# Optimization experiments

Hardware: AMD Instinct MI355X
Metric: run time of the kernel (lower is better)

Reference implementation:

```python
import jax, jax.numpy as jnp
import numpy as np

IN_SIZE = 256
OUT_SIZE = 2


def setup_inputs() -> dict:
    key = jax.random.key(0)
    k1, k2, k3, k4 = jax.random.split(key, 4)
    B, S, D, O = 32, 1024, IN_SIZE, OUT_SIZE
    input1 = jax.random.normal(k1, (B, S, D), dtype=jnp.float32)
    input2 = jax.random.normal(k2, (B, S, D), dtype=jnp.float32)
    # learned parameters
    w1 = jax.random.normal(k3, (D, O, D), dtype=jnp.float32) * 0.02
    w2 = jax.random.normal(k4, (2 * D + 1, O), dtype=jnp.float32) * 0.02
    return {"input1": input1, "input2": input2, "w1": w1, "w2": w2}


def reference(input1, input2, w1, w2):
    D = w1.shape[0]
    # bilinear term: bxi,ioj,byj -> bxyo
    logits1 = jnp.einsum('bxi,ioj,byj->bxyo', input1, w1, input2)
    # linear term: original concat([f1, f2, 1]) @ w2 == input1 @ w2[:D]
    # broadcast over y, plus input2 @ w2[D:2D] broadcast over x, plus bias w2[2D]
    lin1 = jnp.einsum('bxd,do->bxo', input1, w2[:D])        # (B, S, O)
    lin2 = jnp.einsum('byd,do->byo', input2, w2[D:2 * D])   # (B, S, O)
    bias = w2[2 * D]                                        # (O,)
    logits2 = lin1[:, :, None, :] + lin2[:, None, :, :] + bias
    return logits1 + logits2
```

## Files before the change

### kernel.cpp

```cpp
#include <hip/hip_runtime.h>
#include <hip/hip_bf16.h>
#include <cstdint>
#include <cstddef>


typedef __bf16 bf16_t;
typedef __bf16 bf16x4 __attribute__((ext_vector_type(4)));
typedef __bf16 bf16x8 __attribute__((ext_vector_type(8)));
typedef float  f32x4  __attribute__((ext_vector_type(4)));
typedef float  f32x16 __attribute__((ext_vector_type(16)));

#define NB   32
#define NS   1024
#define ND   256
#define NM   (NB * NS)
#define NN1  512

__device__ __forceinline__ void gload_lds16(const void* g, void* l) {
  __builtin_amdgcn_global_load_lds(
      (__attribute__((address_space(1))) void*)g,
      (__attribute__((address_space(3))) void*)l, 16, 0, 0);
}

__global__ __launch_bounds__(256) void prep_kernel(
    const float* __restrict__ in1, const float* __restrict__ in2,
    const float* __restrict__ w1,  const float* __restrict__ w2,
    bf16_t* __restrict__ in1b, bf16_t* __restrict__ in2b,
    bf16_t* __restrict__ w1t,  float* __restrict__ lin)
{
  int bid = blockIdx.x;
  if (bid < 16384) {
    int wave = threadIdx.x >> 6;
    int lane = threadIdx.x & 63;
    int r  = bid * 4 + wave;
    int is2 = (r >= NM) ? 1 : 0;
    int lr = r & (NM - 1);
    const float* src = is2 ? in2 : in1;
    bf16_t*      dst = is2 ? in2b : in1b;

    float4 v = *(const float4*)(src + (size_t)lr * ND + lane * 4);
    bf16x4 h;
    h[0] = (bf16_t)v.x; h[1] = (bf16_t)v.y; h[2] = (bf16_t)v.z; h[3] = (bf16_t)v.w;
    *(bf16x4*)(dst + (size_t)lr * ND + lane * 4) = h;

    int dbase = is2 * ND + lane * 4;
    float a0 = v.x * w2[(dbase + 0) * 2 + 0] + v.y * w2[(dbase + 1) * 2 + 0]
             + v.z * w2[(dbase + 2) * 2 + 0] + v.w * w2[(dbase + 3) * 2 + 0];
    float a1 = v.x * w2[(dbase + 0) * 2 + 1] + v.y * w2[(dbase + 1) * 2 + 1]
             + v.z * w2[(dbase + 2) * 2 + 1] + v.w * w2[(dbase + 3) * 2 + 1];
    #pragma unroll
    for (int off = 32; off > 0; off >>= 1) {
      a0 += __shfl_down(a0, off, 64);
      a1 += __shfl_down(a1, off, 64);
    }
    if (lane == 0) {
      if (is2) { a0 += w2[2 * ND * 2 + 0]; a1 += w2[2 * ND * 2 + 1]; }
      lin[r * 2 + 0] = a0;
      lin[r * 2 + 1] = a1;
    }
  } else {
    int wb = bid - 16384;
    int t  = threadIdx.x;
    #pragma unroll
    for (int e = 0; e < 8; ++e) {
      int q  = wb * 2048 + e * 256 + t;
      int oj = q >> 8;
      int i  = q & 255;
      w1t[q] = (bf16_t)w1[i * NN1 + oj];
    }
  }
}

__global__ __launch_bounds__(256, 3) void gemm1_kernel(
    const bf16_t* __restrict__ A, const bf16_t* __restrict__ Bt,
    bf16_t* __restrict__ T)
{
  __shared__ __align__(16) bf16_t Ap[64 * 256];
  __shared__ __align__(16) bf16_t Bc[2][128 * 32];

  int m0 = blockIdx.x * 64;
  int t = threadIdx.x, lane = t & 63, wid = t >> 6;
  int wm = (wid >> 1) * 32, wn = (wid & 1) * 64;

  #pragma unroll
  for (int i = 0; i < 8; ++i) {
    int unit = i * 256 + t;
    int row = unit >> 5;
    int c   = unit & 31;
    int cs  = c ^ (row & 7);
    gload_lds16(A + (size_t)(m0 + row) * ND + cs * 8, (char*)Ap + unit * 16);
  }
  #pragma unroll
  for (int i = 0; i < 2; ++i) {
    int unit = i * 256 + t;
    int row = unit >> 2, c = unit & 3, cs = c ^ (row & 3);
    gload_lds16(Bt + (size_t)row * ND + cs * 8, (char*)Bc[0] + unit * 16);
  }
  __syncthreads();

  f32x4 acc[2][4] = {};

  for (int s = 0; s < 32; ++s) {
    if (s + 1 < 32) {
      int nt = (s + 1) >> 3, j0 = ((s + 1) & 7) * 32;
      bf16_t* dst = (bf16_t*)Bc[(s + 1) & 1];
      #pragma unroll
      for (int i = 0; i < 2; ++i) {
        int unit = i * 256 + t;
        int row = unit >> 2, c = unit & 3, cs = c ^ (row & 3);
        gload_lds16(Bt + (size_t)(nt * 128 + row) * ND + j0 + cs * 8,
                    (char*)dst + unit * 16);
      }
    }
    const bf16_t* Bcur = Bc[s & 1];
    bf16x8 bfr[4];
    #pragma unroll
    for (int ni = 0; ni < 4; ++ni) {
      int r = wn + ni * 16 + (lane & 15);
      int cp = (lane >> 4) ^ (r & 3);
      bfr[ni] = *(const bf16x8*)&Bcur[r * 32 + cp * 8];
    }
    #pragma unroll
    for (int mi = 0; mi < 2; ++mi) {
      int r = wm + mi * 16 + (lane & 15);
      int cl = (s & 7) * 4 + (lane >> 4);
      int cp = cl ^ (r & 7);
      bf16x8 af = *(const bf16x8*)&Ap[r * 256 + cp * 8];
      #pragma unroll
      for (int ni = 0; ni < 4; ++ni)
        acc[mi][ni] = __builtin_amdgcn_mfma_f32_16x16x32_bf16(
            af, bfr[ni], acc[mi][ni], 0, 0, 0);
    }
    if ((s & 7) == 7) {
      int nt = s >> 3;
      #pragma unroll
      for (int mi = 0; mi < 2; ++mi) {
        int row = m0 + wm + mi * 16 + ((lane >> 4) << 2);
        #pragma unroll
        for (int ni = 0; ni < 4; ++ni) {
          int col = nt * 128 + wn + ni * 16 + (lane & 15);
          #pragma unroll
          for (int r_ = 0; r_ < 4; ++r_)
            T[(size_t)(row + r_) * NN1 + col] = (bf16_t)acc[mi][ni][r_];
          acc[mi][ni] = (f32x4){0.f, 0.f, 0.f, 0.f};
        }
      }
    }
    __syncthreads();
  }
}

__global__ __launch_bounds__(256, 2) void gemm2_kernel(
    const bf16_t* __restrict__ Tm, const bf16_t* __restrict__ in2b,
    const float* __restrict__ lin, float* __restrict__ out)
{
  __shared__ __align__(16) char smem[65536];
  bf16_t* Ap = (bf16_t*)smem;
  bf16_t* Bbuf[2] = { (bf16_t*)smem, (bf16_t*)(smem + 16384) };

  int blk = (blockIdx.x & 7) * 64 + (blockIdx.x >> 3);
  int b   = blk >> 4;
  int x0  = (blk & 15) * 64;
  const bf16_t* Tb = Tm   + (size_t)b * NS * NN1;
  const bf16_t* Ib = in2b + (size_t)b * NS * ND;

  int t = threadIdx.x, lane = t & 63, wid = t >> 6;
  int wx = (wid >> 1) * 32;
  int wy = (wid & 1) * 64;
  int l31 = lane & 31, lhi = lane >> 5;

  #pragma unroll
  for (int i = 0; i < 16; ++i) {
    int unit = i * 256 + t;
    int row = unit >> 6;
    int c   = unit & 63;
    int cs  = c ^ (row & 7);
    gload_lds16(Tb + (size_t)(x0 + row) * NN1 + cs * 8, (char*)Ap + unit * 16);
  }
  __syncthreads();

  bf16x8 af[2][16];
  {
    int row = wx + l31;
    #pragma unroll
    for (int o = 0; o < 2; ++o)
      #pragma unroll
      for (int ks = 0; ks < 16; ++ks) {
        int ls = o * 32 + ks * 2 + lhi;
        int sm = ls ^ (row & 7);
        af[o][ks] = *(const bf16x8*)&Ap[(row * 64 + sm) * 8];
      }
  }
  __syncthreads();

  #pragma unroll
  for (int i = 0; i < 4; ++i) {
    int u = i * 256 + t;
    int row = u >> 3, sm = u & 7;
    int cs = sm ^ (row & 7);
    gload_lds16(Ib + (size_t)row * ND + cs * 8, (char*)Bbuf[0] + u * 16);
  }
  __syncthreads();

  f32x16 acc[2][2] = {};
  float2* outb = (float2*)(out + (size_t)b * NS * NS * 2);
  const float2* l1p = (const float2*)(lin + (size_t)b * NS * 2);
  const float2* l2p = (const float2*)(lin + (size_t)(NM + b * NS) * 2);

  for (int yi = 0; yi < 8; ++yi) {
    #pragma unroll
    for (int kc = 0; kc < 4; ++kc) {
      if (yi < 7 || kc < 3) {
        int c1 = yi * 4 + kc + 1;
        int yn = c1 >> 2, kn = (c1 & 3) * 64;
        char* dst = (char*)Bbuf[(kc + 1) & 1];
        #pragma unroll
        for (int i = 0; i < 4; ++i) {
          int u = i * 256 + t;
          int row = u >> 3, sm = u & 7;
          int cs = sm ^ (row & 7);
          gload_lds16(Ib + (size_t)(yn * 128 + row) * ND + kn + cs * 8,
                      dst + u * 16);
        }
      }
      const bf16_t* Bp = Bbuf[kc & 1];
      #pragma unroll
      for (int ni = 0; ni < 2; ++ni) {
        int row = wy + ni * 32 + l31;
        #pragma unroll
        for (int k2 = 0; k2 < 4; ++k2) {
          int ls = k2 * 2 + lhi;
          int sm = ls ^ (row & 7);
          bf16x8 bf = *(const bf16x8*)&Bp[(row * 8 + sm) * 8];
          acc[ni][0] = __builtin_amdgcn_mfma_f32_32x32x16_bf16(
              af[0][kc * 4 + k2], bf, acc[ni][0], 0, 0, 0);
          acc[ni][1] = __builtin_amdgcn_mfma_f32_32x32x16_bf16(
              af[1][kc * 4 + k2], bf, acc[ni][1], 0, 0, 0);
        }
      }
      if (kc == 3) {
        int y0 = yi * 128;
        float2 l2[2];
        #pragma unroll
        for (int ni = 0; ni < 2; ++ni) l2[ni] = l2p[y0 + wy + ni * 32 + l31];
        int xr = x0 + wx + 4 * lhi;
        #pragma unroll
        for (int r = 0; r < 16; ++r) {
          int row = xr + (r & 3) + 8 * (r >> 2);
          float2 l1 = l1p[row];
          #pragma unroll
          for (int ni = 0; ni < 2; ++ni) {
            int col = y0 + wy + ni * 32 + l31;
            float2 v;
            v.x = acc[ni][0][r] + l1.x + l2[ni].x;
            v.y = acc[ni][1][r] + l1.y + l2[ni].y;
            outb[(size_t)row * NS + col] = v;
          }
        }
        acc[0][0] = (f32x16)(0.f); acc[0][1] = (f32x16)(0.f);
        acc[1][0] = (f32x16)(0.f); acc[1][1] = (f32x16)(0.f);
      }
      __syncthreads();
    }
  }
}

extern "C" void kernel_launch(void* const* d_in, const int* in_sizes, int n_in,
                              void* d_out, int out_size, void* d_ws, size_t ws_size,
                              hipStream_t stream) {
  const float* in1 = (const float*)d_in[0];
  const float* in2 = (const float*)d_in[1];
  const float* w1  = (const float*)d_in[2];
  const float* w2  = (const float*)d_in[3];
  float* out = (float*)d_out;

  char* ws = (char*)d_ws;
  bf16_t* in1b = (bf16_t*)(ws);
  bf16_t* in2b = (bf16_t*)(ws + (16u << 20));
  bf16_t* w1t  = (bf16_t*)(ws + (32u << 20));
  float*  lin  = (float*) (ws + (32u << 20) + (256u << 10));
  bf16_t* T    = (bf16_t*)(ws + (33u << 20));

  prep_kernel<<<16448, 256, 0, stream>>>(in1, in2, w1, w2, in1b, in2b, w1t, lin);
  gemm1_kernel<<<512, 256, 0, stream>>>(in1b, w1t, T);
  gemm2_kernel<<<512, 256, 0, stream>>>(T, in2b, lin, out);
}
```

Baseline: 118.3 us.

## Fold linear terms into MFMA tail and deepen gemm2 B-tile pipeline

New measurement: 161.2 us. 1.36x slower.

```diff
diff --git a/kernel.cpp b/kernel.cpp
--- a/kernel.cpp
+++ b/kernel.cpp
@@ -22,11 +22,21 @@
       (__attribute__((address_space(3))) void*)l, 16, 0, 0);
 }
 
+__device__ __forceinline__ unsigned int bfbits(float f) {
+  unsigned int u = __builtin_bit_cast(unsigned int, f);
+  u += 0x7fffu + ((u >> 16) & 1u);
+  return u >> 16;
+}
+__device__ __forceinline__ bf16_t bf_frombits(unsigned short u) {
+  union { unsigned short s; bf16_t b; } v; v.s = u; return v.b;
+}
+
 __global__ __launch_bounds__(256) void prep_kernel(
     const float* __restrict__ in1, const float* __restrict__ in2,
     const float* __restrict__ w1,  const float* __restrict__ w2,
     bf16_t* __restrict__ in1b, bf16_t* __restrict__ in2b,
-    bf16_t* __restrict__ w1t,  float* __restrict__ lin)
+    bf16_t* __restrict__ w1t,  unsigned int* __restrict__ lin1bf,
+    bf16_t* __restrict__ btail)
 {
   int bid = blockIdx.x;
   if (bid < 16384) {
@@ -54,9 +64,17 @@
       a1 += __shfl_down(a1, off, 64);
     }
     if (lane == 0) {
-      if (is2) { a0 += w2[2 * ND * 2 + 0]; a1 += w2[2 * ND * 2 + 1]; }
-      lin[r * 2 + 0] = a0;
-      lin[r * 2 + 1] = a1;
+      if (is2) {
+        a0 += w2[2 * ND * 2 + 0]; a1 += w2[2 * ND * 2 + 1];
+        unsigned int w0 = 0x3F80u | (bfbits(a0) << 16);
+        unsigned int w1v = bfbits(a1);
+        uint4* p = (uint4*)(btail + (size_t)lr * 16);
+        uint4 z0; z0.x = w0; z0.y = w1v; z0.z = 0u; z0.w = 0u;
+        uint4 z1; z1.x = 0u; z1.y = 0u; z1.z = 0u; z1.w = 0u;
+        p[0] = z0; p[1] = z1;
+      } else {
+        lin1bf[lr] = bfbits(a0) | (bfbits(a1) << 16);
+      }
     }
   } else {
     int wb = bid - 16384;
@@ -152,23 +170,26 @@
 
 __global__ __launch_bounds__(256, 2) void gemm2_kernel(
     const bf16_t* __restrict__ Tm, const bf16_t* __restrict__ in2b,
-    const float* __restrict__ lin, float* __restrict__ out)
+    const unsigned int* __restrict__ lin1bf, const bf16_t* __restrict__ btail,
+    float* __restrict__ out)
 {
-  __shared__ __align__(16) char smem[65536];
-  bf16_t* Ap = (bf16_t*)smem;
-  bf16_t* Bbuf[2] = { (bf16_t*)smem, (bf16_t*)(smem + 16384) };
+  __shared__ __align__(16) char smem_all[73728];
+  char* smem    = smem_all;
+  char* tailmem = smem_all + 65536;
 
   int blk = (blockIdx.x & 7) * 64 + (blockIdx.x >> 3);
   int b   = blk >> 4;
   int x0  = (blk & 15) * 64;
-  const bf16_t* Tb = Tm   + (size_t)b * NS * NN1;
-  const bf16_t* Ib = in2b + (size_t)b * NS * ND;
+  const bf16_t* Tb  = Tm    + (size_t)b * NS * NN1;
+  const bf16_t* Ib  = in2b  + (size_t)b * NS * ND;
+  const bf16_t* Btg = btail + (size_t)b * NS * 16;
 
   int t = threadIdx.x, lane = t & 63, wid = t >> 6;
   int wx = (wid >> 1) * 32;
   int wy = (wid & 1) * 64;
   int l31 = lane & 31, lhi = lane >> 5;
 
+  bf16_t* Ap = (bf16_t*)smem;
   #pragma unroll
   for (int i = 0; i < 16; ++i) {
     int unit = i * 256 + t;
@@ -193,76 +214,105 @@
   }
   __syncthreads();
 
-  #pragma unroll
-  for (int i = 0; i < 4; ++i) {
-    int u = i * 256 + t;
-    int row = u >> 3, sm = u & 7;
-    int cs = sm ^ (row & 7);
-    gload_lds16(Ib + (size_t)row * ND + cs * 8, (char*)Bbuf[0] + u * 16);
-  }
-  __syncthreads();
+  unsigned int lv = lin1bf[(size_t)b * NS + x0 + wx + l31];
+  bf16x8 aft0 = {}, aft1 = {};
+  if (lhi == 0) {
+    aft0[0] = bf_frombits((unsigned short)(lv & 0xffffu));
+    aft0[1] = bf_frombits(0x3F80u);
+    aft1[0] = bf_frombits((unsigned short)(lv >> 16));
+    aft1[2] = bf_frombits(0x3F80u);
+  }
 
   f32x16 acc[2][2] = {};
   float2* outb = (float2*)(out + (size_t)b * NS * NS * 2);
-  const float2* l1p = (const float2*)(lin + (size_t)b * NS * 2);
-  const float2* l2p = (const float2*)(lin + (size_t)(NM + b * NS) * 2);
-
-  for (int yi = 0; yi < 8; ++yi) {
-    #pragma unroll
-    for (int kc = 0; kc < 4; ++kc) {
-      if (yi < 7 || kc < 3) {
-        int c1 = yi * 4 + kc + 1;
-        int yn = c1 >> 2, kn = (c1 & 3) * 64;
-        char* dst = (char*)Bbuf[(kc + 1) & 1];
-        #pragma unroll
-        for (int i = 0; i < 4; ++i) {
-          int u = i * 256 + t;
-          int row = u >> 3, sm = u & 7;
-          int cs = sm ^ (row & 7);
-          gload_lds16(Ib + (size_t)(yn * 128 + row) * ND + kn + cs * 8,
-                      dst + u * 16);
-        }
-      }
-      const bf16_t* Bp = Bbuf[kc & 1];
-      #pragma unroll
-      for (int ni = 0; ni < 2; ++ni) {
-        int row = wy + ni * 32 + l31;
-        #pragma unroll
-        for (int k2 = 0; k2 < 4; ++k2) {
-          int ls = k2 * 2 + lhi;
-          int sm = ls ^ (row & 7);
-          bf16x8 bf = *(const bf16x8*)&Bp[(row * 8 + sm) * 8];
-          acc[ni][0] = __builtin_amdgcn_mfma_f32_32x32x16_bf16(
-              af[0][kc * 4 + k2], bf, acc[ni][0], 0, 0, 0);
-          acc[ni][1] = __builtin_amdgcn_mfma_f32_32x32x16_bf16(
-              af[1][kc * 4 + k2], bf, acc[ni][1], 0, 0, 0);
-        }
-      }
-      if (kc == 3) {
-        int y0 = yi * 128;
-        float2 l2[2];
-        #pragma unroll
-        for (int ni = 0; ni < 2; ++ni) l2[ni] = l2p[y0 + wy + ni * 32 + l31];
-        int xr = x0 + wx + 4 * lhi;
-        #pragma unroll
-        for (int r = 0; r < 16; ++r) {
-          int row = xr + (r & 3) + 8 * (r >> 2);
-          float2 l1 = l1p[row];
-          #pragma unroll
-          for (int ni = 0; ni < 2; ++ni) {
-            int col = y0 + wy + ni * 32 + l31;
-            float2 v;
-            v.x = acc[ni][0][r] + l1.x + l2[ni].x;
-            v.y = acc[ni][1][r] + l1.y + l2[ni].y;
-            outb[(size_t)row * NS + col] = v;
-          }
-        }
-        acc[0][0] = (f32x16)(0.f); acc[0][1] = (f32x16)(0.f);
-        acc[1][0] = (f32x16)(0.f); acc[1][1] = (f32x16)(0.f);
-      }
-      __syncthreads();
-    }
-  }
+  int xr = x0 + wx + 4 * lhi;
+
+#define G2_ISSUE(YI2, KC2) do {                                               \
+    char* dst_ = smem + (KC2) * 16384;                                        \
+    _Pragma("unroll")                                                         \
+    for (int i_ = 0; i_ < 4; ++i_) {                                          \
+      int u_ = i_ * 256 + t;                                                  \
+      int row_ = u_ >> 3, sm_ = u_ & 7;                                       \
+      int cs_ = sm_ ^ (row_ & 7);                                             \
+      gload_lds16(Ib + (size_t)((YI2) * 128 + row_) * ND + (KC2) * 64 + cs_ * 8, \
+                  dst_ + u_ * 16);                                            \
+    }                                                                         \
+    if ((KC2) == 3) {                                                         \
+      char* td_ = tailmem + ((YI2) & 1) * 4096;                               \
+      int row_ = t >> 1, h_ = t & 1;                                          \
+      gload_lds16(Btg + (size_t)((YI2) * 128 + row_) * 16 + h_ * 8,           \
+                  td_ + t * 16);                                              \
+    }                                                                         \
+  } while (0)
+
+#define G2_STEP(YI, KC, WN, DO_ISSUE) do {                                    \
+    if (DO_ISSUE) G2_ISSUE((YI) + ((KC) >= 2 ? 1 : 0), ((KC) + 2) & 3);       \
+    asm volatile("s_waitcnt vmcnt(" #WN ")" ::: "memory");                    \
+    __builtin_amdgcn_sched_barrier(0);                                        \
+    __builtin_amdgcn_s_barrier();                                             \
+    __builtin_amdgcn_sched_barrier(0);                                        \
+    const bf16_t* Bp_ = (const bf16_t*)(smem + (KC) * 16384);                 \
+    _Pragma("unroll")                                                         \
+    for (int ni_ = 0; ni_ < 2; ++ni_) {                                       \
+      int row_ = wy + ni_ * 32 + l31;                                         \
+      _Pragma("unroll")                                                       \
+      for (int k2_ = 0; k2_ < 4; ++k2_) {                                     \
+        int ls_ = k2_ * 2 + lhi;                                              \
+        int sm_ = ls_ ^ (row_ & 7);                                           \
+        bf16x8 bf_ = *(const bf16x8*)&Bp_[(row_ * 8 + sm_) * 8];              \
+        acc[ni_][0] = __builtin_amdgcn_mfma_f32_32x32x16_bf16(                \
+            af[0][(KC) * 4 + k2_], bf_, acc[ni_][0], 0, 0, 0);                \
+        acc[ni_][1] = __builtin_amdgcn_mfma_f32_32x32x16_bf16(                \
+            af[1][(KC) * 4 + k2_], bf_, acc[ni_][1], 0, 0, 0);                \
+      }                                                                       \
+    }                                                                         \
+    if ((KC) == 3) {                                                          \
+      const bf16_t* Tp_ = (const bf16_t*)(tailmem + ((YI) & 1) * 4096);       \
+      _Pragma("unroll")                                                       \
+      for (int ni_ = 0; ni_ < 2; ++ni_) {                                     \
+        int row_ = wy + ni_ * 32 + l31;                                       \
+        bf16x8 bt_ = *(const bf16x8*)&Tp_[row_ * 16 + lhi * 8];               \
+        acc[ni_][0] = __builtin_amdgcn_mfma_f32_32x32x16_bf16(                \
+            aft0, bt_, acc[ni_][0], 0, 0, 0);                                 \
+        acc[ni_][1] = __builtin_amdgcn_mfma_f32_32x32x16_bf16(                \
+            aft1, bt_, acc[ni_][1], 0, 0, 0);                                 \
+      }                                                                       \
+      int y0_ = (YI) * 128;                                                   \
+      _Pragma("unroll")                                                       \
+      for (int r_ = 0; r_ < 16; ++r_) {                                       \
+        int row_ = xr + (r_ & 3) + 8 * (r_ >> 2);                             \
+        _Pragma("unroll")                                                     \
+        for (int ni_ = 0; ni_ < 2; ++ni_) {                                   \
+          int col_ = y0_ + wy + ni_ * 32 + l31;                               \
+          float2 v_; v_.x = acc[ni_][0][r_]; v_.y = acc[ni_][1][r_];          \
+          outb[(size_t)row_ * NS + col_] = v_;                                \
+        }                                                                     \
+      }                                                                       \
+      acc[0][0] = (f32x16)(0.f); acc[0][1] = (f32x16)(0.f);                   \
+      acc[1][0] = (f32x16)(0.f); acc[1][1] = (f32x16)(0.f);                   \
+    }                                                                         \
+  } while (0)
+
+  G2_ISSUE(0, 0);
+  G2_ISSUE(0, 1);
+
+  G2_STEP(0, 0, 8, true);
+  G2_STEP(0, 1, 9, true);
+  G2_STEP(0, 2, 9, true);
+  G2_STEP(0, 3, 8, true);
+  for (int yi = 1; yi < 7; ++yi) {
+    G2_STEP(yi, 0, 40, true);
+    G2_STEP(yi, 1, 41, true);
+    G2_STEP(yi, 2, 9, true);
+    G2_STEP(yi, 3, 8, true);
+  }
+  G2_STEP(7, 0, 40, true);
+  G2_STEP(7, 1, 41, true);
+  G2_STEP(7, 2, 5, false);
+  G2_STEP(7, 3, 0, false);
+
+#undef G2_STEP
+#undef G2_ISSUE
 }
 
 extern "C" void kernel_launch(void* const* d_in, const int* in_sizes, int n_in,
@@ -275,13 +325,15 @@
   float* out = (float*)d_out;
 
   char* ws = (char*)d_ws;
-  bf16_t* in1b = (bf16_t*)(ws);
-  bf16_t* in2b = (bf16_t*)(ws + (16u << 20));
-  bf16_t* w1t  = (bf16_t*)(ws + (32u << 20));
-  float*  lin  = (float*) (ws + (32u << 20) + (256u << 10));
-  bf16_t* T    = (bf16_t*)(ws + (33u << 20));
-
-  prep_kernel<<<16448, 256, 0, stream>>>(in1, in2, w1, w2, in1b, in2b, w1t, lin);
+  bf16_t*       in1b   = (bf16_t*)(ws);
+  bf16_t*       in2b   = (bf16_t*)(ws + (16u << 20));
+  bf16_t*       w1t    = (bf16_t*)(ws + (32u << 20));
+  unsigned int* lin1bf = (unsigned int*)(ws + (32u << 20) + (256u << 10));
+  bf16_t*       btail  = (bf16_t*)(ws + (32u << 20) + (512u << 10));
+  bf16_t*       T      = (bf16_t*)(ws + (34u << 20));
+
+  prep_kernel<<<16448, 256, 0, stream>>>(in1, in2, w1, w2, in1b, in2b, w1t,
+                                         lin1bf, btail);
   gemm1_kernel<<<512, 256, 0, stream>>>(in1b, w1t, T);
-  gemm2_kernel<<<512, 256, 0, stream>>>(T, in2b, lin, out);
-}
+  gemm2_kernel<<<512, 256, 0, stream>>>(T, in2b, lin1bf, btail, out);
+}
```

## Enlarge gemm2 tiles to 128 rows and stage full-K B panels

Applied to the files above, without the earlier changes.

Measured after the change: 150.1 us. 1.27x slower.

```diff
diff --git a/kernel.cpp b/kernel.cpp
--- a/kernel.cpp
+++ b/kernel.cpp
@@ -150,17 +150,15 @@
   }
 }
 
-__global__ __launch_bounds__(256, 2) void gemm2_kernel(
+__global__ __launch_bounds__(512, 2) void gemm2_kernel(
     const bf16_t* __restrict__ Tm, const bf16_t* __restrict__ in2b,
     const float* __restrict__ lin, float* __restrict__ out)
 {
-  __shared__ __align__(16) char smem[65536];
-  bf16_t* Ap = (bf16_t*)smem;
-  bf16_t* Bbuf[2] = { (bf16_t*)smem, (bf16_t*)(smem + 16384) };
-
-  int blk = (blockIdx.x & 7) * 64 + (blockIdx.x >> 3);
-  int b   = blk >> 4;
-  int x0  = (blk & 15) * 64;
+  __shared__ __align__(16) char smem[131072];
+
+  int blk = (blockIdx.x & 7) * 32 + (blockIdx.x >> 3);
+  int b   = blk >> 3;
+  int x0  = (blk & 7) * 128;
   const bf16_t* Tb = Tm   + (size_t)b * NS * NN1;
   const bf16_t* Ib = in2b + (size_t)b * NS * ND;
 
@@ -169,13 +167,14 @@
   int wy = (wid & 1) * 64;
   int l31 = lane & 31, lhi = lane >> 5;
 
+  bf16_t* Apan = (bf16_t*)smem;
   #pragma unroll
   for (int i = 0; i < 16; ++i) {
-    int unit = i * 256 + t;
+    int unit = i * 512 + t;
     int row = unit >> 6;
     int c   = unit & 63;
     int cs  = c ^ (row & 7);
-    gload_lds16(Tb + (size_t)(x0 + row) * NN1 + cs * 8, (char*)Ap + unit * 16);
+    gload_lds16(Tb + (size_t)(x0 + row) * NN1 + cs * 8, (char*)Apan + unit * 16);
   }
   __syncthreads();
 
@@ -188,17 +187,17 @@
       for (int ks = 0; ks < 16; ++ks) {
         int ls = o * 32 + ks * 2 + lhi;
         int sm = ls ^ (row & 7);
-        af[o][ks] = *(const bf16x8*)&Ap[(row * 64 + sm) * 8];
-      }
-  }
-  __syncthreads();
-
-  #pragma unroll
-  for (int i = 0; i < 4; ++i) {
-    int u = i * 256 + t;
-    int row = u >> 3, sm = u & 7;
-    int cs = sm ^ (row & 7);
-    gload_lds16(Ib + (size_t)row * ND + cs * 8, (char*)Bbuf[0] + u * 16);
+        af[o][ks] = *(const bf16x8*)&Apan[(row * 64 + sm) * 8];
+      }
+  }
+  __syncthreads();
+
+  #pragma unroll
+  for (int i = 0; i < 8; ++i) {
+    int u = i * 512 + t;
+    int row = u >> 5, sl = u & 31;
+    int cs = sl ^ (row & 7);
+    gload_lds16(Ib + (size_t)row * ND + cs * 8, smem + u * 16);
   }
   __syncthreads();
 
@@ -206,62 +205,57 @@
   float2* outb = (float2*)(out + (size_t)b * NS * NS * 2);
   const float2* l1p = (const float2*)(lin + (size_t)b * NS * 2);
   const float2* l2p = (const float2*)(lin + (size_t)(NM + b * NS) * 2);
-
-  for (int yi = 0; yi < 8; ++yi) {
-    #pragma unroll
-    for (int kc = 0; kc < 4; ++kc) {
-      if (yi < 7 || kc < 3) {
-        int c1 = yi * 4 + kc + 1;
-        int yn = c1 >> 2, kn = (c1 & 3) * 64;
-        char* dst = (char*)Bbuf[(kc + 1) & 1];
-        #pragma unroll
-        for (int i = 0; i < 4; ++i) {
-          int u = i * 256 + t;
-          int row = u >> 3, sm = u & 7;
-          int cs = sm ^ (row & 7);
-          gload_lds16(Ib + (size_t)(yn * 128 + row) * ND + kn + cs * 8,
-                      dst + u * 16);
-        }
-      }
-      const bf16_t* Bp = Bbuf[kc & 1];
+  int xr = x0 + wx + 4 * lhi;
+
+  for (int p = 0; p < 8; ++p) {
+    if (p + 1 < 8) {
+      char* dst = smem + ((p + 1) & 1) * 65536;
+      #pragma unroll
+      for (int i = 0; i < 8; ++i) {
+        int u = i * 512 + t;
+        int row = u >> 5, sl = u & 31;
+        int cs = sl ^ (row & 7);
+        gload_lds16(Ib + (size_t)((p + 1) * 128 + row) * ND + cs * 8,
+                    dst + u * 16);
+      }
+    }
+    const bf16_t* Bp = (const bf16_t*)(smem + (p & 1) * 65536);
+    #pragma unroll
+    for (int ks = 0; ks < 16; ++ks) {
       #pragma unroll
       for (int ni = 0; ni < 2; ++ni) {
         int row = wy + ni * 32 + l31;
+        int ls = ks * 2 + lhi;
+        int sm = ls ^ (row & 7);
+        bf16x8 bfv = *(const bf16x8*)&Bp[(row * 32 + sm) * 8];
+        acc[ni][0] = __builtin_amdgcn_mfma_f32_32x32x16_bf16(
+            af[0][ks], bfv, acc[ni][0], 0, 0, 0);
+        acc[ni][1] = __builtin_amdgcn_mfma_f32_32x32x16_bf16(
+            af[1][ks], bfv, acc[ni][1], 0, 0, 0);
+      }
+    }
+    {
+      int y0 = p * 128;
+      float2 l2[2];
+      #pragma unroll
+      for (int ni = 0; ni < 2; ++ni) l2[ni] = l2p[y0 + wy + ni * 32 + l31];
+      #pragma unroll
+      for (int r = 0; r < 16; ++r) {
+        int row = xr + (r & 3) + 8 * (r >> 2);
+        float2 l1 = l1p[row];
         #pragma unroll
-        for (int k2 = 0; k2 < 4; ++k2) {
-          int ls = k2 * 2 + lhi;
-          int sm = ls ^ (row & 7);
-          bf16x8 bf = *(const bf16x8*)&Bp[(row * 8 + sm) * 8];
-          acc[ni][0] = __builtin_amdgcn_mfma_f32_32x32x16_bf16(
-              af[0][kc * 4 + k2], bf, acc[ni][0], 0, 0, 0);
-          acc[ni][1] = __builtin_amdgcn_mfma_f32_32x32x16_bf16(
-              af[1][kc * 4 + k2], bf, acc[ni][1], 0, 0, 0);
+        for (int ni = 0; ni < 2; ++ni) {
+          int col = y0 + wy + ni * 32 + l31;
+          float2 v;
+          v.x = acc[ni][0][r] + l1.x + l2[ni].x;
+          v.y = acc[ni][1][r] + l1.y + l2[ni].y;
+          outb[(size_t)row * NS + col] = v;
         }
       }
-      if (kc == 3) {
-        int y0 = yi * 128;
-        float2 l2[2];
-        #pragma unroll
-        for (int ni = 0; ni < 2; ++ni) l2[ni] = l2p[y0 + wy + ni * 32 + l31];
-        int xr = x0 + wx + 4 * lhi;
-        #pragma unroll
-        for (int r = 0; r < 16; ++r) {
-          int row = xr + (r & 3) + 8 * (r >> 2);
-          float2 l1 = l1p[row];
-          #pragma unroll
-          for (int ni = 0; ni < 2; ++ni) {
-            int col = y0 + wy + ni * 32 + l31;
-            float2 v;
-            v.x = acc[ni][0][r] + l1.x + l2[ni].x;
-            v.y = acc[ni][1][r] + l1.y + l2[ni].y;
-            outb[(size_t)row * NS + col] = v;
-          }
-        }
-        acc[0][0] = (f32x16)(0.f); acc[0][1] = (f32x16)(0.f);
-        acc[1][0] = (f32x16)(0.f); acc[1][1] = (f32x16)(0.f);
-      }
-      __syncthreads();
-    }
+      acc[0][0] = (f32x16)(0.f); acc[0][1] = (f32x16)(0.f);
+      acc[1][0] = (f32x16)(0.f); acc[1][1] = (f32x16)(0.f);
+    }
+    __syncthreads();
   }
 }
 
@@ -283,5 +277,5 @@
 
   prep_kernel<<<16448, 256, 0, stream>>>(in1, in2, w1, w2, in1b, in2b, w1t, lin);
   gemm1_kernel<<<512, 256, 0, stream>>>(in1b, w1t, T);
-  gemm2_kernel<<<512, 256, 0, stream>>>(T, in2b, lin, out);
-}
+  gemm2_kernel<<<256, 512, 0, stream>>>(T, in2b, lin, out);
+}
```
